# Performance work log

Measured on AMD Instinct MI355X. Metric: run time of the kernel, lower is better.

## Reference

```python
import jax, jax.numpy as jnp
import numpy as np

NEG_INF = -9e15  # matches torch's -9000000000000000.0 mask value
LEAKY_SLOPE = 0.2  # init alpha


def setup_inputs() -> dict:
    key = jax.random.key(0)
    k1, k2, k3, k4 = jax.random.split(key, 4)
    N, dim = 4096, 128
    hidden = jax.random.normal(k1, (N, dim), dtype=jnp.float32)
    adj = jax.random.randint(k2, (N, N), 0, 5)  # relation codes 0..4
    W = jax.random.normal(k3, (4, dim), dtype=jnp.float32) * (1.0 / np.sqrt(dim))
    b = jax.random.normal(k4, (4,), dtype=jnp.float32) * 0.01
    return {"hidden": hidden, "adj": adj, "W": W, "b": b}


def reference(hidden, adj, W, b):
    # e_k[i,j] = leakyrelu(sum_d h[i,d]*h[j,d]*W[k,d] + b[k])
    # equivalent to the torch repeat/view outer-product + four dim->1 Linears,
    # computed without materializing the [N,N,dim] intermediate.
    hw = hidden[None, :, :] * W[:, None, :]               # [4, N, dim]
    e = jnp.einsum('knd,md->knm', hw, hidden) + b[:, None, None]  # [4, N, N]
    e = jax.nn.leaky_relu(e, negative_slope=LEAKY_SLOPE)
    neg = jnp.asarray(NEG_INF, dtype=e.dtype)
    alpha = jnp.where(adj == 1, e[0], neg)
    alpha = jnp.where(adj == 2, e[1], alpha)
    alpha = jnp.where(adj == 3, e[2], alpha)
    alpha = jnp.where(adj == 4, e[3], alpha)
    alpha = jax.nn.softmax(alpha, axis=-1)                # [N, N]
    return alpha @ hidden                                  # [N, dim]
```

## Files before the change

kernel.cpp:

```cpp
#include <hip/hip_runtime.h>

#define NN 4096
#define DIM 128
#define TN 64
#define TM 128
#define NSPLIT 4
#define NTILES 8

typedef __attribute__((ext_vector_type(8))) short bf16x8;
typedef __attribute__((ext_vector_type(4))) float f32x4;

#define LSTRIDE 136
#define REGION  (128 * LSTRIDE)
#define TILE_USH (2 * REGION)
#define TILE_CHUNKS 68
#define PST 136

__device__ inline unsigned short f2bf(float x) {
    union { float f; unsigned u; } v; v.f = x;
    unsigned r = v.u + 0x7FFFu + ((v.u >> 16) & 1u);
    return (unsigned short)(r >> 16);
}

__device__ inline void dma16(const void* g, void* l) {
    __builtin_amdgcn_global_load_lds(
        (const __attribute__((address_space(1))) void*)g,
        (__attribute__((address_space(3))) void*)l,
        16, 0, 0);
}

__global__ __launch_bounds__(256) void prep_pack_kernel(
    const float* __restrict__ hidden,
    unsigned short* __restrict__ Hpack)
{
    __shared__ unsigned short T[16][LSTRIDE];
    const int tid = threadIdx.x;
    const int t0  = blockIdx.x >> 3;
    const int s   = blockIdx.x & 7;
    const int m0  = t0 * TM;
    unsigned short* rowdst = Hpack + (size_t)t0 * TILE_USH;
    unsigned short* coldst = rowdst + REGION;

    #pragma unroll
    for (int it = 0; it < 2; ++it) {
        int idx = tid + 256 * it;
        int row = idx >> 5;
        int c4  = (idx & 31) * 4;
        float4 v = *(const float4*)(hidden + (size_t)(m0 + 16 * s + row) * DIM + c4);
        ushort4 o;
        o.x = f2bf(v.x); o.y = f2bf(v.y); o.z = f2bf(v.z); o.w = f2bf(v.w);
        *(ushort4*)(rowdst + (16 * s + row) * LSTRIDE + c4) = o;
    }
    #pragma unroll
    for (int it = 0; it < 2; ++it) {
        int idx = tid + 256 * it;
        int m  = idx >> 2;
        int dc = (idx & 3) * 4;
        float4 v = *(const float4*)(hidden + (size_t)(m0 + m) * DIM + 16 * s + dc);
        T[dc + 0][m] = f2bf(v.x);
        T[dc + 1][m] = f2bf(v.y);
        T[dc + 2][m] = f2bf(v.z);
        T[dc + 3][m] = f2bf(v.w);
    }
    __syncthreads();
    {
        int d  = tid >> 4;
        int c8 = (tid & 15) * 8;
        uint4 v = *(const uint4*)(&T[d][c8]);
        *(uint4*)(coldst + (16 * s + d) * LSTRIDE + c8) = v;
    }
}

__global__ __launch_bounds__(1024, 4) void gat_flash_kernel(
    const float* __restrict__ hidden,
    const unsigned short* __restrict__ Hpack,
    const int*   __restrict__ adj,
    const float* __restrict__ W,
    const float* __restrict__ bvec,
    float*       __restrict__ Opart,
    float*       __restrict__ lpart)
{
    __shared__ __align__(16) unsigned short HH[2][TILE_USH];
    __shared__ __align__(16) unsigned short Plc[TN * PST];
    __shared__ float redsum[16][16];

    const int tid  = threadIdx.x;
    const int w    = tid >> 6;
    const int lane = tid & 63;
    const int g    = lane >> 4;
    const int l15  = lane & 15;
    const int blk  = blockIdx.x;
    const int nbr  = blk >> 2;
    const int q4   = blk & 3;
    const int n0   = nbr * TN;
    const int gt0  = q4 * NTILES;
    const int rg   = w >> 2;
    const int msw  = w & 3;
    const int lofs = lane * 16;

    const float b0 = bvec[0], b1 = bvec[1], b2 = bvec[2], b3 = bvec[3];

    {
        const char* src = (const char*)(Hpack + (size_t)gt0 * TILE_USH);
        char* dst = (char*)&HH[0][0];
        #pragma unroll
        for (int it = 0; it < 5; ++it) {
            int chunk = it * 16 + w;
            if (chunk < TILE_CHUNKS)
                dma16(src + chunk * 1024 + lofs, dst + chunk * 1024);
        }
    }
    {
        #pragma unroll
        for (int it = 0; it < 2; ++it) {
            int idx = tid + 1024 * it;
            int row = idx >> 3;
            int c16 = (idx & 7) * 16;
            int k = row >> 6, r = row & 63;
            const float* hrow = hidden + (size_t)(n0 + r) * DIM + c16;
            const float* wrow = W + k * DIM + c16;
            unsigned short* qdst = &HH[1][row * LSTRIDE + c16];
            #pragma unroll
            for (int c = 0; c < 4; ++c) {
                float4 hv = *(const float4*)(hrow + 4 * c);
                float4 wv = *(const float4*)(wrow + 4 * c);
                ushort4 o;
                o.x = f2bf(hv.x * wv.x); o.y = f2bf(hv.y * wv.y);
                o.z = f2bf(hv.z * wv.z); o.w = f2bf(hv.w * wv.w);
                *(ushort4*)(qdst + 4 * c) = o;
            }
        }
    }
    __syncthreads();

    bf16x8 Af[4][4];
    #pragma unroll
    for (int k = 0; k < 4; ++k)
        #pragma unroll
        for (int ks = 0; ks < 4; ++ks)
            Af[k][ks] = *(const bf16x8*)&HH[1][(k * 64 + rg * 16 + l15) * LSTRIDE + ks * 32 + 8 * g];
    __syncthreads();

    float lrow[4] = {0.f, 0.f, 0.f, 0.f};
    f32x4 Oacc[2];
    #pragma unroll
    for (int dt = 0; dt < 2; ++dt) Oacc[dt] = (f32x4){0.f, 0.f, 0.f, 0.f};

    const size_t arow = (size_t)(n0 + rg * 16 + 4 * g) * NN;
    int avc[8], avn[8];
    #pragma unroll
    for (int ch = 0; ch < 2; ++ch)
        #pragma unroll
        for (int t = 0; t < 4; ++t)
            avc[ch * 4 + t] = adj[arow + (size_t)t * NN + gt0 * TM + msw * 32 + ch * 16 + l15];

    for (int tile = 0; tile < NTILES; ++tile) {
        const int cur = tile & 1;
        const int nxt = cur ^ 1;

        if (tile + 1 < NTILES) {
            const char* src = (const char*)(Hpack + (size_t)(gt0 + tile + 1) * TILE_USH);
            char* dst = (char*)&HH[nxt][0];
            #pragma unroll
            for (int it = 0; it < 5; ++it) {
                int chunk = it * 16 + w;
                if (chunk < TILE_CHUNKS)
                    dma16(src + chunk * 1024 + lofs, dst + chunk * 1024);
            }
        }

        #pragma unroll
        for (int ch = 0; ch < 2; ++ch) {
            f32x4 S[4];
            #pragma unroll
            for (int k = 0; k < 4; ++k) S[k] = (f32x4){0.f, 0.f, 0.f, 0.f};
            #pragma unroll
            for (int ks = 0; ks < 4; ++ks) {
                bf16x8 B = *(const bf16x8*)&HH[cur][(msw * 32 + ch * 16 + l15) * LSTRIDE + ks * 32 + 8 * g];
                #pragma unroll
                for (int k = 0; k < 4; ++k)
                    S[k] = __builtin_amdgcn_mfma_f32_16x16x32_bf16(Af[k][ks], B, S[k], 0, 0, 0);
            }
            #pragma unroll
            for (int t = 0; t < 4; ++t) {
                int a = avc[ch * 4 + t];
                float s = S[0][t] + b0;
                s = (a == 2) ? S[1][t] + b1 : s;
                s = (a == 3) ? S[2][t] + b2 : s;
                s = (a == 4) ? S[3][t] + b3 : s;
                float e = fmaxf(s, 0.2f * s);
                float p = __expf(e);
                p = (a == 0) ? 0.f : p;
                lrow[t] += p;
                Plc[(rg * 16 + 4 * g + t) * PST + msw * 32 + ch * 16 + l15] = f2bf(p);
            }
        }

        if (tile + 1 < NTILES) {
            #pragma unroll
            for (int ch = 0; ch < 2; ++ch)
                #pragma unroll
                for (int t = 0; t < 4; ++t)
                    avn[ch * 4 + t] = adj[arow + (size_t)t * NN + (size_t)(gt0 + tile + 1) * TM + msw * 32 + ch * 16 + l15];
        }

        asm volatile("s_waitcnt lgkmcnt(0)\n\ts_barrier" ::: "memory");

        #pragma unroll
        for (int c4 = 0; c4 < 4; ++c4) {
            bf16x8 Pa = *(const bf16x8*)&Plc[(rg * 16 + l15) * PST + c4 * 32 + 8 * g];
            #pragma unroll
            for (int dt = 0; dt < 2; ++dt) {
                bf16x8 Bv = *(const bf16x8*)&HH[cur][REGION + (msw * 32 + dt * 16 + l15) * LSTRIDE + c4 * 32 + 8 * g];
                Oacc[dt] = __builtin_amdgcn_mfma_f32_16x16x32_bf16(Pa, Bv, Oacc[dt], 0, 0, 0);
            }
        }

        #pragma unroll
        for (int i = 0; i < 8; ++i) avc[i] = avn[i];
        __syncthreads();
    }

    #pragma unroll
    for (int t = 0; t < 4; ++t) {
        float v = lrow[t];
        v += __shfl_xor(v, 1); v += __shfl_xor(v, 2);
        v += __shfl_xor(v, 4); v += __shfl_xor(v, 8);
        if (l15 == 0) redsum[w][4 * g + t] = v;
    }
    __syncthreads();
    if (tid < TN) {
        int rg2 = tid >> 4, rr = tid & 15;
        lpart[blk * TN + tid] = redsum[rg2 * 4 + 0][rr] + redsum[rg2 * 4 + 1][rr]
                              + redsum[rg2 * 4 + 2][rr] + redsum[rg2 * 4 + 3][rr];
    }
    float* Ob = Opart + (size_t)blk * (TN * DIM);
    #pragma unroll
    for (int dt = 0; dt < 2; ++dt)
        #pragma unroll
        for (int t = 0; t < 4; ++t)
            Ob[(rg * 16 + 4 * g + t) * DIM + msw * 32 + dt * 16 + l15] = Oacc[dt][t];
}

__global__ __launch_bounds__(256) void combine_kernel(
    const float* __restrict__ Opart, const float* __restrict__ lpart,
    float* __restrict__ out)
{
    int idx = blockIdx.x * 256 + threadIdx.x;
    int r = idx >> 7, d = idx & 127;
    int nbr = r >> 6, rr = r & 63;
    float O = 0.f, l = 0.f;
    #pragma unroll
    for (int q = 0; q < NSPLIT; ++q) {
        O += Opart[(size_t)(nbr * NSPLIT + q) * (TN * DIM) + rr * 128 + d];
        l += lpart[(nbr * NSPLIT + q) * TN + rr];
    }
    out[idx] = O / l;
}

extern "C" void kernel_launch(void* const* d_in, const int* in_sizes, int n_in,
                              void* d_out, int out_size, void* d_ws, size_t ws_size,
                              hipStream_t stream) {
    const float* hidden = (const float*)d_in[0];
    const int*   adj    = (const int*)d_in[1];
    const float* W      = (const float*)d_in[2];
    const float* b      = (const float*)d_in[3];
    float* out = (float*)d_out;

    char* ws = (char*)d_ws;
    unsigned short* Hpack = (unsigned short*)ws;
    float* Opart = (float*)(ws + (4u << 20));
    float* lpart = (float*)(ws + (12u << 20));

    prep_pack_kernel<<<(NN / TM) * 8, 256, 0, stream>>>(hidden, Hpack);
    gat_flash_kernel<<<256, 1024, 0, stream>>>(hidden, Hpack, adj, W, b, Opart, lpart);
    combine_kernel<<<NN * DIM / 256, 256, 0, stream>>>(Opart, lpart, out);
}
```

Measured before the change: 147.0 us.

## Halve row and column tile sizes, doubling block count with 512 threads

Reduces the query-row tile from 64 to 32 and the key tile from 128 to 64, so the flash kernel launches 512 blocks of 512 threads instead of 256 blocks of 1024. The packed H layout, LDS strides, prep kernel and combine kernel are rewritten for the smaller tiles. The aim is more blocks across the CUs and a smaller LDS footprint per block for better occupancy and latency hiding. The cost is lower data reuse per tile, more tile iterations with barriers, and more DMA traffic relative to compute.

```diff
diff --git a/kernel.cpp b/kernel.cpp
--- a/kernel.cpp
+++ b/kernel.cpp
@@ -2,19 +2,21 @@
 
 #define NN 4096
 #define DIM 128
-#define TN 64
-#define TM 128
+#define TN 32
+#define TM 64
 #define NSPLIT 4
-#define NTILES 8
+#define NTILES 16
 
 typedef __attribute__((ext_vector_type(8))) short bf16x8;
 typedef __attribute__((ext_vector_type(4))) float f32x4;
 
-#define LSTRIDE 136
-#define REGION  (128 * LSTRIDE)
-#define TILE_USH (2 * REGION)
-#define TILE_CHUNKS 68
-#define PST 136
+#define HRS 136
+#define HCS 72
+#define HROW_USH (TM * HRS)
+#define HCOL_USH (128 * HCS)
+#define TILE_USH (HROW_USH + HCOL_USH)
+#define TILE_CHUNKS 35
+#define PST 72
 
 __device__ inline unsigned short f2bf(float x) {
     union { float f; unsigned u; } v; v.f = x;
@@ -33,29 +35,25 @@
     const float* __restrict__ hidden,
     unsigned short* __restrict__ Hpack)
 {
-    __shared__ unsigned short T[16][LSTRIDE];
+    __shared__ unsigned short T[16][HCS];
     const int tid = threadIdx.x;
     const int t0  = blockIdx.x >> 3;
     const int s   = blockIdx.x & 7;
     const int m0  = t0 * TM;
     unsigned short* rowdst = Hpack + (size_t)t0 * TILE_USH;
-    unsigned short* coldst = rowdst + REGION;
-
-    #pragma unroll
-    for (int it = 0; it < 2; ++it) {
-        int idx = tid + 256 * it;
-        int row = idx >> 5;
-        int c4  = (idx & 31) * 4;
-        float4 v = *(const float4*)(hidden + (size_t)(m0 + 16 * s + row) * DIM + c4);
+    unsigned short* coldst = rowdst + HROW_USH;
+
+    {
+        int row = tid >> 5;
+        int c4  = (tid & 31) * 4;
+        float4 v = *(const float4*)(hidden + (size_t)(m0 + 8 * s + row) * DIM + c4);
         ushort4 o;
         o.x = f2bf(v.x); o.y = f2bf(v.y); o.z = f2bf(v.z); o.w = f2bf(v.w);
-        *(ushort4*)(rowdst + (16 * s + row) * LSTRIDE + c4) = o;
-    }
-    #pragma unroll
-    for (int it = 0; it < 2; ++it) {
-        int idx = tid + 256 * it;
-        int m  = idx >> 2;
-        int dc = (idx & 3) * 4;
+        *(ushort4*)(rowdst + (8 * s + row) * HRS + c4) = o;
+    }
+    {
+        int m  = tid >> 2;
+        int dc = (tid & 3) * 4;
         float4 v = *(const float4*)(hidden + (size_t)(m0 + m) * DIM + 16 * s + dc);
         T[dc + 0][m] = f2bf(v.x);
         T[dc + 1][m] = f2bf(v.y);
@@ -63,15 +61,15 @@
         T[dc + 3][m] = f2bf(v.w);
     }
     __syncthreads();
-    {
-        int d  = tid >> 4;
-        int c8 = (tid & 15) * 8;
+    if (tid < 128) {
+        int d  = tid >> 3;
+        int c8 = (tid & 7) * 8;
         uint4 v = *(const uint4*)(&T[d][c8]);
-        *(uint4*)(coldst + (16 * s + d) * LSTRIDE + c8) = v;
-    }
-}
-
-__global__ __launch_bounds__(1024, 4) void gat_flash_kernel(
+        *(uint4*)(coldst + (16 * s + d) * HCS + c8) = v;
+    }
+}
+
+__global__ __launch_bounds__(512, 4) void gat_flash_kernel(
     const float* __restrict__ hidden,
     const unsigned short* __restrict__ Hpack,
     const int*   __restrict__ adj,
@@ -82,7 +80,7 @@
 {
     __shared__ __align__(16) unsigned short HH[2][TILE_USH];
     __shared__ __align__(16) unsigned short Plc[TN * PST];
-    __shared__ float redsum[16][16];
+    __shared__ float redsum[8][16];
 
     const int tid  = threadIdx.x;
     const int w    = tid >> 6;
@@ -97,6 +95,8 @@
     const int rg   = w >> 2;
     const int msw  = w & 3;
     const int lofs = lane * 16;
+    const float NEG = -9.0e15f;
+    (void)NEG;
 
     const float b0 = bvec[0], b1 = bvec[1], b2 = bvec[2], b3 = bvec[3];
 
@@ -105,7 +105,7 @@
         char* dst = (char*)&HH[0][0];
         #pragma unroll
         for (int it = 0; it < 5; ++it) {
-            int chunk = it * 16 + w;
+            int chunk = it * 8 + w;
             if (chunk < TILE_CHUNKS)
                 dma16(src + chunk * 1024 + lofs, dst + chunk * 1024);
         }
@@ -113,13 +113,13 @@
     {
         #pragma unroll
         for (int it = 0; it < 2; ++it) {
-            int idx = tid + 1024 * it;
+            int idx = tid + 512 * it;
             int row = idx >> 3;
             int c16 = (idx & 7) * 16;
-            int k = row >> 6, r = row & 63;
+            int k = row >> 5, r = row & 31;
             const float* hrow = hidden + (size_t)(n0 + r) * DIM + c16;
             const float* wrow = W + k * DIM + c16;
-            unsigned short* qdst = &HH[1][row * LSTRIDE + c16];
+            unsigned short* qdst = &HH[1][row * HRS + c16];
             #pragma unroll
             for (int c = 0; c < 4; ++c) {
                 float4 hv = *(const float4*)(hrow + 4 * c);
@@ -138,7 +138,7 @@
     for (int k = 0; k < 4; ++k)
         #pragma unroll
         for (int ks = 0; ks < 4; ++ks)
-            Af[k][ks] = *(const bf16x8*)&HH[1][(k * 64 + rg * 16 + l15) * LSTRIDE + ks * 32 + 8 * g];
+            Af[k][ks] = *(const bf16x8*)&HH[1][(k * 32 + rg * 16 + l15) * HRS + ks * 32 + 8 * g];
     __syncthreads();
 
     float lrow[4] = {0.f, 0.f, 0.f, 0.f};
@@ -147,12 +147,10 @@
     for (int dt = 0; dt < 2; ++dt) Oacc[dt] = (f32x4){0.f, 0.f, 0.f, 0.f};
 
     const size_t arow = (size_t)(n0 + rg * 16 + 4 * g) * NN;
-    int avc[8], avn[8];
-    #pragma unroll
-    for (int ch = 0; ch < 2; ++ch)
-        #pragma unroll
-        for (int t = 0; t < 4; ++t)
-            avc[ch * 4 + t] = adj[arow + (size_t)t * NN + gt0 * TM + msw * 32 + ch * 16 + l15];
+    int avc[4], avn[4];
+    #pragma unroll
+    for (int t = 0; t < 4; ++t)
+        avc[t] = adj[arow + (size_t)t * NN + gt0 * TM + msw * 16 + l15];
 
     for (int tile = 0; tile < NTILES; ++tile) {
         const int cur = tile & 1;
@@ -163,61 +161,57 @@
             char* dst = (char*)&HH[nxt][0];
             #pragma unroll
             for (int it = 0; it < 5; ++it) {
-                int chunk = it * 16 + w;
+                int chunk = it * 8 + w;
                 if (chunk < TILE_CHUNKS)
                     dma16(src + chunk * 1024 + lofs, dst + chunk * 1024);
             }
         }
 
-        #pragma unroll
-        for (int ch = 0; ch < 2; ++ch) {
-            f32x4 S[4];
-            #pragma unroll
-            for (int k = 0; k < 4; ++k) S[k] = (f32x4){0.f, 0.f, 0.f, 0.f};
-            #pragma unroll
-            for (int ks = 0; ks < 4; ++ks) {
-                bf16x8 B = *(const bf16x8*)&HH[cur][(msw * 32 + ch * 16 + l15) * LSTRIDE + ks * 32 + 8 * g];
-                #pragma unroll
-                for (int k = 0; k < 4; ++k)
-                    S[k] = __builtin_amdgcn_mfma_f32_16x16x32_bf16(Af[k][ks], B, S[k], 0, 0, 0);
-            }
-            #pragma unroll
-            for (int t = 0; t < 4; ++t) {
-                int a = avc[ch * 4 + t];
-                float s = S[0][t] + b0;
-                s = (a == 2) ? S[1][t] + b1 : s;
-                s = (a == 3) ? S[2][t] + b2 : s;
-                s = (a == 4) ? S[3][t] + b3 : s;
-                float e = fmaxf(s, 0.2f * s);
-                float p = __expf(e);
-                p = (a == 0) ? 0.f : p;
-                lrow[t] += p;
-                Plc[(rg * 16 + 4 * g + t) * PST + msw * 32 + ch * 16 + l15] = f2bf(p);
-            }
+        f32x4 S[4];
+        #pragma unroll
+        for (int k = 0; k < 4; ++k) S[k] = (f32x4){0.f, 0.f, 0.f, 0.f};
+        #pragma unroll
+        for (int ks = 0; ks < 4; ++ks) {
+            bf16x8 B = *(const bf16x8*)&HH[cur][(msw * 16 + l15) * HRS + ks * 32 + 8 * g];
+            #pragma unroll
+            for (int k = 0; k < 4; ++k)
+                S[k] = __builtin_amdgcn_mfma_f32_16x16x32_bf16(Af[k][ks], B, S[k], 0, 0, 0);
+        }
+
+        #pragma unroll
+        for (int t = 0; t < 4; ++t) {
+            int a = avc[t];
+            float s = S[0][t] + b0;
+            s = (a == 2) ? S[1][t] + b1 : s;
+            s = (a == 3) ? S[2][t] + b2 : s;
+            s = (a == 4) ? S[3][t] + b3 : s;
+            float e = fmaxf(s, 0.2f * s);
+            float p = __expf(e);
+            p = (a == 0) ? 0.f : p;
+            lrow[t] += p;
+            Plc[(rg * 16 + 4 * g + t) * PST + msw * 16 + l15] = f2bf(p);
         }
 
         if (tile + 1 < NTILES) {
             #pragma unroll
-            for (int ch = 0; ch < 2; ++ch)
-                #pragma unroll
-                for (int t = 0; t < 4; ++t)
-                    avn[ch * 4 + t] = adj[arow + (size_t)t * NN + (size_t)(gt0 + tile + 1) * TM + msw * 32 + ch * 16 + l15];
+            for (int t = 0; t < 4; ++t)
+                avn[t] = adj[arow + (size_t)t * NN + (size_t)(gt0 + tile + 1) * TM + msw * 16 + l15];
         }
 
         asm volatile("s_waitcnt lgkmcnt(0)\n\ts_barrier" ::: "memory");
 
         #pragma unroll
-        for (int c4 = 0; c4 < 4; ++c4) {
-            bf16x8 Pa = *(const bf16x8*)&Plc[(rg * 16 + l15) * PST + c4 * 32 + 8 * g];
+        for (int kc = 0; kc < 2; ++kc) {
+            bf16x8 Pa = *(const bf16x8*)&Plc[(rg * 16 + l15) * PST + kc * 32 + 8 * g];
             #pragma unroll
             for (int dt = 0; dt < 2; ++dt) {
-                bf16x8 Bv = *(const bf16x8*)&HH[cur][REGION + (msw * 32 + dt * 16 + l15) * LSTRIDE + c4 * 32 + 8 * g];
+                bf16x8 Bv = *(const bf16x8*)&HH[cur][HROW_USH + (msw * 32 + dt * 16 + l15) * HCS + kc * 32 + 8 * g];
                 Oacc[dt] = __builtin_amdgcn_mfma_f32_16x16x32_bf16(Pa, Bv, Oacc[dt], 0, 0, 0);
             }
         }
 
         #pragma unroll
-        for (int i = 0; i < 8; ++i) avc[i] = avn[i];
+        for (int i = 0; i < 4; ++i) avc[i] = avn[i];
         __syncthreads();
     }
 
@@ -248,7 +242,7 @@
 {
     int idx = blockIdx.x * 256 + threadIdx.x;
     int r = idx >> 7, d = idx & 127;
-    int nbr = r >> 6, rr = r & 63;
+    int nbr = r >> 5, rr = r & 31;
     float O = 0.f, l = 0.f;
     #pragma unroll
     for (int q = 0; q < NSPLIT; ++q) {
@@ -273,6 +267,6 @@
     float* lpart = (float*)(ws + (12u << 20));
 
     prep_pack_kernel<<<(NN / TM) * 8, 256, 0, stream>>>(hidden, Hpack);
-    gat_flash_kernel<<<256, 1024, 0, stream>>>(hidden, Hpack, adj, W, b, Opart, lpart);
+    gat_flash_kernel<<<512, 512, 0, stream>>>(hidden, Hpack, adj, W, b, Opart, lpart);
     combine_kernel<<<NN * DIM / 256, 256, 0, stream>>>(Opart, lpart, out);
 }
```

After: 138.9 us. 1.06x faster.
